# Kernel optimization log

Measured on AMD Instinct MI355X. Metric: run time of the kernel, lower is better.

Reference implementation:

```python
import jax, jax.numpy as jnp
import numpy as np

T, B, NS, NC = 100, 4096, 12, 4
N = NS + NC  # tau dim


def setup_inputs() -> dict:
    key = jax.random.key(0)
    k1, k2, k3, k4, k5 = jax.random.split(key, 5)
    # Symmetric PD quadratic cost C = L L^T / N + I  -> well conditioned
    L = jax.random.normal(k1, (T, B, N, N), dtype=jnp.float32) * 0.1
    C = jnp.einsum('tbij,tbkj->tbik', L, L) + jnp.eye(N, dtype=jnp.float32)
    c = jax.random.normal(k2, (T, B, N), dtype=jnp.float32)
    # Linear dynamics x' = F [x;u] + f, state block near identity for stability
    F = jax.random.normal(k3, (T - 1, B, NS, N), dtype=jnp.float32) * 0.02
    A0 = jnp.concatenate([0.99 * jnp.eye(NS, dtype=jnp.float32),
                          jnp.zeros((NS, NC), jnp.float32)], axis=-1)
    F = F + A0  # broadcast over (T-1, B)
    f = jax.random.normal(k4, (T - 1, B, NS), dtype=jnp.float32) * 0.01
    x_init = jax.random.normal(k5, (B, NS), dtype=jnp.float32)
    return {"x_init": x_init, "C": C, "c": c, "F": F, "f": f}


def _lqr_solve(x_init, C, c, F, f):
    ns = x_init.shape[-1]
    # Pad dynamics to length T (terminal step has no dynamics; V starts at 0
    # so the padded zero F/f contribute nothing).
    Fp = jnp.concatenate([F, jnp.zeros_like(F[:1])], axis=0)  # [T,B,ns,n]
    fp = jnp.concatenate([f, jnp.zeros_like(f[:1])], axis=0)  # [T,B,ns]

    def bwd_step(carry, inp):
        V, v = carry                      # [B,ns,ns], [B,ns]
        Ct, ct, Ft, ft = inp
        # Q = C + F^T V F ; q = c + F^T (V f + v)
        Q = Ct + jnp.einsum('bsi,bst,btj->bij', Ft, V, Ft)
        Vf = jnp.einsum('bst,bt->bs', V, ft) + v
        q = ct + jnp.einsum('bsi,bs->bi', Ft, Vf)
        Qxx, Qxu = Q[:, :ns, :ns], Q[:, :ns, ns:]
        Qux, Quu = Q[:, ns:, :ns], Q[:, ns:, ns:]
        qx, qu = q[:, :ns], q[:, ns:]
        # Joint solve for K = -Quu^{-1} Qux, k = -Quu^{-1} qu
        Kk = -jnp.linalg.solve(Quu, jnp.concatenate([Qux, qu[..., None]], axis=-1))
        K, k = Kk[..., :ns], Kk[..., ns]
        Vn = Qxx + jnp.einsum('bij,bjk->bik', Qxu, K)
        Vn = 0.5 * (Vn + jnp.swapaxes(Vn, -1, -2))
        vn = qx + jnp.einsum('bij,bj->bi', Qxu, k)
        return (Vn, vn), (K, k)

    V0 = jnp.zeros((x_init.shape[0], ns, ns), C.dtype)
    v0 = jnp.zeros((x_init.shape[0], ns), C.dtype)
    _, (Kr, kr) = jax.lax.scan(bwd_step, (V0, v0),
                               (C[::-1], c[::-1], Fp[::-1], fp[::-1]))
    K, k = Kr[::-1], kr[::-1]  # [T,B,nc,ns], [T,B,nc]

    def fwd_step(x, inp):
        Ct, ct, Ft, ft, Kt, kt = inp
        u = jnp.einsum('bij,bj->bi', Kt, x) + kt
        tau = jnp.concatenate([x, u], axis=-1)
        cost = 0.5 * jnp.einsum('bi,bij,bj->b', tau, Ct, tau) \
               + jnp.einsum('bi,bi->b', ct, tau)
        xn = jnp.einsum('bij,bj->bi', Ft, tau) + ft
        return xn, (x, u, cost)

    _, (xs, us, costs) = jax.lax.scan(fwd_step, x_init, (C, c, Fp, fp, K, k))
    return xs, us, jnp.sum(costs, axis=0)


def reference(x_init, C, c, F, f):
    # MPC with QuadCost + LinDx and no box constraints: the iLQR loop
    # converges in one exact LQR solve (Riccati backward + forward rollout).
    x, u, objs = _lqr_solve(x_init, C, c, F, f)
    return x, u, objs
```

## Files before the change

### kernel.cpp

```cpp
#include <hip/hip_runtime.h>
#include <hip/hip_fp16.h>

#define TT 100
#define BB 4096
#define GS 648


__device__ __forceinline__ void bar_lds(){
  asm volatile("" ::: "memory");
  asm volatile("s_waitcnt lgkmcnt(0)" ::: "memory");
  __builtin_amdgcn_s_barrier();
  asm volatile("" ::: "memory");
}

template<int KMODE>
__device__ __forceinline__ void storeK(void* wsv, size_t of, int l, float X0,float X1,float X2,float X3){
  if (KMODE==0){
    float* wsb=(float*)wsv + of*52;
    if (l<12)       ((float4*)wsb)[l]  = make_float4(X0,X1,X2,X3);
    else if (l==12) ((float4*)wsb)[12] = make_float4(X0,X1,X2,X3);
  } else {
    __half* wsb=(__half*)wsv + of*52;
    if (l<12){
      wsb[l*4+0]=__float2half(X0); wsb[l*4+1]=__float2half(X1);
      wsb[l*4+2]=__float2half(X2); wsb[l*4+3]=__float2half(X3);
    } else if (l==12){
      wsb[48]=__float2half(X0); wsb[49]=__float2half(X1);
      wsb[50]=__float2half(X2); wsb[51]=__float2half(X3);
    }
  }
}
template<int KMODE>
__device__ __forceinline__ float4 loadKcol(const void* wsv, size_t of, int l){
  if (KMODE==0) return ((const float4*)((const float*)wsv + of*52))[l];
  const __half* p=(const __half*)wsv + of*52 + l*4;
  return make_float4(__half2float(p[0]),__half2float(p[1]),__half2float(p[2]),__half2float(p[3]));
}
template<int KMODE>
__device__ __forceinline__ float loadkk(const void* wsv, size_t of, int r){
  if (KMODE==0) return ((const float*)wsv)[of*52+48+r];
  return __half2float(((const __half*)wsv)[of*52+48+r]);
}

template<int KMODE>
__global__ __launch_bounds__(256)
void lqr_fused(const float* __restrict__ xinit,
               const float* __restrict__ Cg,
               const float* __restrict__ cg,
               const float* __restrict__ Fg,
               const float* __restrict__ fg,
               float* __restrict__ out,
               void* __restrict__ wsv)
{
  __shared__ float smem[GS*16];
  const int tid = threadIdx.x;
  const int g = tid >> 4, l = tid & 15;
  const int b = blockIdx.x*16 + g;
  const int gb = (tid & 63) & ~15;

  float* __restrict__ V   = smem + (size_t)g*GS;
  float* __restrict__ Fl  = V + 144;
  float* __restrict__ S   = V + 384;
  float* __restrict__ Qxu = V + 528;
  float* __restrict__ Quu = V + 576;
  float* __restrict__ vv  = V + 592;
  float* __restrict__ tb  = V + 604;

  if (l < 12){
    #pragma unroll
    for (int i=0;i<12;i++) V[i*12+l]=0.f;
    vv[l]=0.f;
  }

  float4 sC0,sC1,sC2,sC3; float sc_;
  float4 sF0=make_float4(0,0,0,0),sF1=sF0,sF2=sF0,sF3=sF0; float sf_=0.f;
  {
    const size_t of = ((size_t)(TT-1)*BB + b);
    const float4* pc = (const float4*)(Cg + of*256 + l*16);
    sC0=pc[0];sC1=pc[1];sC2=pc[2];sC3=pc[3];
    sc_ = cg[of*16 + l];
  }

  for (int tt=TT-1; tt>=0; --tt){
    const bool hasF = (tt < TT-1);
    float4 C0=sC0,C1=sC1,C2=sC2,C3=sC3; float rc=sc_;
    float4 F0=sF0,F1=sF1,F2=sF2,F3=sF3; float rf=sf_;

    if (hasF && l<12){
      float4* q=(float4*)(Fl + l*20);
      q[0]=F0;q[1]=F1;q[2]=F2;q[3]=F3;
      tb[l]=rf;
    }
    bar_lds();

    if (tt>0){
      const size_t of = ((size_t)(tt-1)*BB + b);
      const float4* pc=(const float4*)(Cg + of*256 + l*16);
      sC0=pc[0];sC1=pc[1];sC2=pc[2];sC3=pc[3];
      sc_=cg[of*16+l];
      if (l<12){
        const float4* pf=(const float4*)(Fg + of*192 + l*16);
        sF0=pf[0];sF1=pf[1];sF2=pf[2];sF3=pf[3];
        sf_=fg[of*12+l];
      }
    }

    float Qc[16] = {C0.x,C0.y,C0.z,C0.w, C1.x,C1.y,C1.z,C1.w,
                    C2.x,C2.y,C2.z,C2.w, C3.x,C3.y,C3.z,C3.w};
    float qv = rc;

    if (hasF){
      float Ftj[12], W[12];
      #pragma unroll
      for (int s=0;s<12;s++) Ftj[s]=Fl[s*20+l];
      #pragma unroll
      for (int s=0;s<12;s++){
        const float4* vr=(const float4*)(V+s*12);
        float4 v0=vr[0],v1=vr[1],v2=vr[2];
        W[s]= v0.x*Ftj[0]+v0.y*Ftj[1]+v0.z*Ftj[2]+v0.w*Ftj[3]
            + v1.x*Ftj[4]+v1.y*Ftj[5]+v1.z*Ftj[6]+v1.w*Ftj[7]
            + v2.x*Ftj[8]+v2.y*Ftj[9]+v2.z*Ftj[10]+v2.w*Ftj[11];
      }
      #pragma unroll
      for (int s=0;s<12;s++){
        const float4* fr=(const float4*)(Fl + s*20);
        float4 f0=fr[0],f1=fr[1],f2=fr[2],f3=fr[3];
        float w=W[s];
        Qc[0]+=f0.x*w;  Qc[1]+=f0.y*w;  Qc[2]+=f0.z*w;  Qc[3]+=f0.w*w;
        Qc[4]+=f1.x*w;  Qc[5]+=f1.y*w;  Qc[6]+=f1.z*w;  Qc[7]+=f1.w*w;
        Qc[8]+=f2.x*w;  Qc[9]+=f2.y*w;  Qc[10]+=f2.z*w; Qc[11]+=f2.w*w;
        Qc[12]+=f3.x*w; Qc[13]+=f3.y*w; Qc[14]+=f3.z*w; Qc[15]+=f3.w*w;
      }
      #pragma unroll
      for (int t2=0;t2<12;t2++) qv += W[t2]*tb[t2];
      #pragma unroll
      for (int s=0;s<12;s++) qv += Ftj[s]*vv[s];
    }

    if (l>=12){
      const int cc=l-12;
      #pragma unroll
      for (int r=0;r<4;r++) Quu[cc*4+r]=Qc[12+r];
      #pragma unroll
      for (int i=0;i<12;i++) Qxu[cc*12+i]=Qc[i];
    }
    bar_lds();

    float qu0=__shfl(qv,gb+12,64),qu1=__shfl(qv,gb+13,64),
          qu2=__shfl(qv,gb+14,64),qu3=__shfl(qv,gb+15,64);
    float b0,b1,b2,b3;
    if (l<12){b0=-Qc[12];b1=-Qc[13];b2=-Qc[14];b3=-Qc[15];}
    else     {b0=-qu0;b1=-qu1;b2=-qu2;b3=-qu3;}

    float a00=Quu[0],a10=Quu[1],a20=Quu[2],a30=Quu[3];
    float a01=Quu[4],a11=Quu[5],a21=Quu[6],a31=Quu[7];
    float a02=Quu[8],a12=Quu[9],a22=Quu[10],a32=Quu[11];
    float a03=Quu[12],a13=Quu[13],a23=Quu[14],a33=Quu[15];

    float i0=1.0f/a00;
    float m10=a10*i0,m20=a20*i0,m30=a30*i0;
    a11-=m10*a01;a12-=m10*a02;a13-=m10*a03;b1-=m10*b0;
    a21-=m20*a01;a22-=m20*a02;a23-=m20*a03;b2-=m20*b0;
    a31-=m30*a01;a32-=m30*a02;a33-=m30*a03;b3-=m30*b0;
    float i1=1.0f/a11;
    float m21=a21*i1,m31=a31*i1;
    a22-=m21*a12;a23-=m21*a13;b2-=m21*b1;
    a32-=m31*a12;a33-=m31*a13;b3-=m31*b1;
    float i2=1.0f/a22;
    float m32=a32*i2;
    a33-=m32*a23;b3-=m32*b2;
    float X3=b3/a33;
    float X2=(b2-a23*X3)*i2;
    float X1=(b1-a12*X2-a13*X3)*i1;
    float X0=(b0-a01*X1-a02*X2-a03*X3)*i0;

    float k0=__shfl(X0,gb+12,64),k1=__shfl(X1,gb+12,64),
          k2=__shfl(X2,gb+12,64),k3=__shfl(X3,gb+12,64);

    storeK<KMODE>(wsv, (size_t)tt*BB+b, l, X0,X1,X2,X3);

    float Vn[12];
    if (l<12){
      #pragma unroll
      for (int i=0;i<12;i++) Vn[i]=Qc[i];
      #pragma unroll
      for (int r=0;r<4;r++){
        const float Xr=(r==0)?X0:(r==1)?X1:(r==2)?X2:X3;
        const float4* qx=(const float4*)(Qxu+r*12);
        float4 x0=qx[0],x1=qx[1],x2=qx[2];
        Vn[0]+=x0.x*Xr; Vn[1]+=x0.y*Xr; Vn[2]+=x0.z*Xr;  Vn[3]+=x0.w*Xr;
        Vn[4]+=x1.x*Xr; Vn[5]+=x1.y*Xr; Vn[6]+=x1.z*Xr;  Vn[7]+=x1.w*Xr;
        Vn[8]+=x2.x*Xr; Vn[9]+=x2.y*Xr; Vn[10]+=x2.z*Xr; Vn[11]+=x2.w*Xr;
      }
      #pragma unroll
      for (int i=0;i<12;i++) S[i*12+l]=Vn[i];
    }
    bar_lds();

    if (l<12){
      float vn = qv + Qxu[0+l]*k0 + Qxu[12+l]*k1 + Qxu[24+l]*k2 + Qxu[36+l]*k3;
      const float4* sr=(const float4*)(S + l*12);
      float4 r0=sr[0],r1=sr[1],r2=sr[2];
      V[0*12+l]=0.5f*(Vn[0]+r0.x);   V[1*12+l]=0.5f*(Vn[1]+r0.y);
      V[2*12+l]=0.5f*(Vn[2]+r0.z);   V[3*12+l]=0.5f*(Vn[3]+r0.w);
      V[4*12+l]=0.5f*(Vn[4]+r1.x);   V[5*12+l]=0.5f*(Vn[5]+r1.y);
      V[6*12+l]=0.5f*(Vn[6]+r1.z);   V[7*12+l]=0.5f*(Vn[7]+r1.w);
      V[8*12+l]=0.5f*(Vn[8]+r2.x);   V[9*12+l]=0.5f*(Vn[9]+r2.y);
      V[10*12+l]=0.5f*(Vn[10]+r2.z); V[11*12+l]=0.5f*(Vn[11]+r2.w);
      vv[l]=vn;
    }
  }

  asm volatile("s_waitcnt vmcnt(0)" ::: "memory");

  float xj = (l<12)? xinit[(size_t)b*12+l] : 0.f;
  double costacc=0.0;

  float4 sK=make_float4(0,0,0,0); float sk_=0.f;
  {
    const float4* pc=(const float4*)(Cg + (size_t)b*256 + l*16);
    sC0=pc[0];sC1=pc[1];sC2=pc[2];sC3=pc[3];
    sc_=cg[(size_t)b*16+l];
    if (l<12){
      const float4* pf=(const float4*)(Fg + (size_t)b*192 + l*16);
      sF0=pf[0];sF1=pf[1];sF2=pf[2];sF3=pf[3];
      sf_=fg[(size_t)b*12+l];
      sK=loadKcol<KMODE>(wsv,(size_t)b,l);
    } else {
      sk_=loadkk<KMODE>(wsv,(size_t)b,l-12);
    }
  }

  for (int t=0;t<TT;t++){
    float4 C0=sC0,C1=sC1,C2=sC2,C3=sC3; float rc=sc_;
    float4 F0=sF0,F1=sF1,F2=sF2,F3=sF3; float rf=sf_;
    float4 K4=sK; float kl=sk_;

    if (t+1<TT){
      const size_t of=((size_t)(t+1)*BB + b);
      const float4* pc=(const float4*)(Cg + of*256 + l*16);
      sC0=pc[0];sC1=pc[1];sC2=pc[2];sC3=pc[3];
      sc_=cg[of*16+l];
      if (l<12) sK=loadKcol<KMODE>(wsv,of,l);
      else      sk_=loadkk<KMODE>(wsv,of,l-12);
      if (t+1<TT-1 && l<12){
        const float4* pf=(const float4*)(Fg + of*192 + l*16);
        sF0=pf[0];sF1=pf[1];sF2=pf[2];sF3=pf[3];
        sf_=fg[of*12+l];
      }
    }

    float pr0=0.f,pr1=0.f,pr2=0.f,pr3=0.f;
    if (l<12){ pr0=K4.x*xj; pr1=K4.y*xj; pr2=K4.z*xj; pr3=K4.w*xj; }
    #pragma unroll
    for (int m=1;m<16;m<<=1){
      pr0+=__shfl_xor(pr0,m,64); pr1+=__shfl_xor(pr1,m,64);
      pr2+=__shfl_xor(pr2,m,64); pr3+=__shfl_xor(pr3,m,64);
    }
    float tauj;
    if (l<12) tauj=xj;
    else {
      float ur=(l==12)?pr0:(l==13)?pr1:(l==14)?pr2:pr3;
      tauj=ur+kl;
    }
    float* tbuf = tb + (t&1)*16;
    tbuf[l]=tauj;
    bar_lds();

    float4 t0=((const float4*)tbuf)[0], t1v=((const float4*)tbuf)[1],
           t2v=((const float4*)tbuf)[2], t3v=((const float4*)tbuf)[3];

    const float Cr[16]={C0.x,C0.y,C0.z,C0.w,C1.x,C1.y,C1.z,C1.w,
                        C2.x,C2.y,C2.z,C2.w,C3.x,C3.y,C3.z,C3.w};
    const float ta[16]={t0.x,t0.y,t0.z,t0.w,t1v.x,t1v.y,t1v.z,t1v.w,
                        t2v.x,t2v.y,t2v.z,t2v.w,t3v.x,t3v.y,t3v.z,t3v.w};
    float dot=0.f;
    #pragma unroll
    for (int j=0;j<16;j++) dot += Cr[j]*ta[j];
    costacc += (double)(tauj*(0.5f*dot+rc));

    if (l<12) out[(size_t)t*BB*12 + (size_t)b*12 + l] = xj;
    else      out[(size_t)TT*BB*12 + (size_t)t*BB*4 + (size_t)b*4 + (l-12)] = tauj;

    if (t<TT-1 && l<12){
      const float Fr[16]={F0.x,F0.y,F0.z,F0.w,F1.x,F1.y,F1.z,F1.w,
                          F2.x,F2.y,F2.z,F2.w,F3.x,F3.y,F3.z,F3.w};
      float d2=rf;
      #pragma unroll
      for (int j=0;j<16;j++) d2 += Fr[j]*ta[j];
      xj=d2;
    }
  }

  costacc+=__shfl_xor(costacc,1,64); costacc+=__shfl_xor(costacc,2,64);
  costacc+=__shfl_xor(costacc,4,64); costacc+=__shfl_xor(costacc,8,64);
  if (l==0) out[(size_t)TT*BB*16 + b]=(float)costacc;
}

extern "C" void kernel_launch(void* const* d_in, const int* in_sizes, int n_in,
                              void* d_out, int out_size, void* d_ws, size_t ws_size,
                              hipStream_t stream){
  (void)in_sizes; (void)n_in; (void)out_size;
  const float* xinit=(const float*)d_in[0];
  const float* C    =(const float*)d_in[1];
  const float* c    =(const float*)d_in[2];
  const float* F    =(const float*)d_in[3];
  const float* f    =(const float*)d_in[4];
  const size_t need_f32 = (size_t)TT*BB*52*sizeof(float);
  if (ws_size >= need_f32){
    lqr_fused<0><<<dim3(BB/16), dim3(256), 0, stream>>>(xinit,C,c,F,f,(float*)d_out,d_ws);
  } else {
    lqr_fused<1><<<dim3(BB/16), dim3(256), 0, stream>>>(xinit,C,c,F,f,(float*)d_out,d_ws);
  }
}
```

Baseline: 526.0 us.

## Split each batch item across 32 lanes and drop block barriers

Each batch element now gets 32 threads (two halves of 16) instead of 16. The F^T V F work, the Q row products and the V update are split across the halves and combined with cross-half shuffles. The grid doubles, and each wave now holds two batch items whose LDS regions never overlap, so the full s_barrier is replaced by an lgkmcnt wait. This is meant to shorten the serial per-step dependency chain and raise parallelism. In exchange the forward pass leaves half the lanes mostly idle and adds extra shuffles.

```diff
diff --git a/kernel.cpp b/kernel.cpp
--- a/kernel.cpp
+++ b/kernel.cpp
@@ -6,12 +6,7 @@
 #define GS 648
 
 
-__device__ __forceinline__ void bar_lds(){
-  asm volatile("" ::: "memory");
-  asm volatile("s_waitcnt lgkmcnt(0)" ::: "memory");
-  __builtin_amdgcn_s_barrier();
-  asm volatile("" ::: "memory");
-}
+#define FENCE() asm volatile("s_waitcnt lgkmcnt(0)" ::: "memory")
 
 template<int KMODE>
 __device__ __forceinline__ void storeK(void* wsv, size_t of, int l, float X0,float X1,float X2,float X3){
@@ -52,13 +47,16 @@
                float* __restrict__ out,
                void* __restrict__ wsv)
 {
-  __shared__ float smem[GS*16];
-  const int tid = threadIdx.x;
-  const int g = tid >> 4, l = tid & 15;
-  const int b = blockIdx.x*16 + g;
-  const int gb = (tid & 63) & ~15;
-
-  float* __restrict__ V   = smem + (size_t)g*GS;
+  __shared__ float smem[GS*8];
+  const int tid  = threadIdx.x;
+  const int gi   = tid >> 5;
+  const int lane = tid & 63;
+  const int l    = tid & 15;
+  const int h    = (tid >> 4) & 1;
+  const int b    = blockIdx.x*8 + gi;
+  const int gb32 = lane & ~31;
+
+  float* __restrict__ V   = smem + gi*GS;
   float* __restrict__ Fl  = V + 144;
   float* __restrict__ S   = V + 384;
   float* __restrict__ Qxu = V + 528;
@@ -66,88 +64,101 @@
   float* __restrict__ vv  = V + 592;
   float* __restrict__ tb  = V + 604;
 
-  if (l < 12){
+  if (h==0 && l<12){
     #pragma unroll
     for (int i=0;i<12;i++) V[i*12+l]=0.f;
     vv[l]=0.f;
   }
 
-  float4 sC0,sC1,sC2,sC3; float sc_;
-  float4 sF0=make_float4(0,0,0,0),sF1=sF0,sF2=sF0,sF3=sF0; float sf_=0.f;
+  float4 sCa,sCb; float sc_;
+  float4 sFa=make_float4(0,0,0,0),sFb=sFa; float sf_=0.f;
   {
     const size_t of = ((size_t)(TT-1)*BB + b);
     const float4* pc = (const float4*)(Cg + of*256 + l*16);
-    sC0=pc[0];sC1=pc[1];sC2=pc[2];sC3=pc[3];
+    sCa=pc[2*h]; sCb=pc[2*h+1];
     sc_ = cg[of*16 + l];
   }
 
   for (int tt=TT-1; tt>=0; --tt){
     const bool hasF = (tt < TT-1);
-    float4 C0=sC0,C1=sC1,C2=sC2,C3=sC3; float rc=sc_;
-    float4 F0=sF0,F1=sF1,F2=sF2,F3=sF3; float rf=sf_;
+    float4 Ca=sCa,Cb=sCb; float rc=sc_;
+    float4 Fa=sFa,Fb=sFb; float rf=sf_;
 
     if (hasF && l<12){
       float4* q=(float4*)(Fl + l*20);
-      q[0]=F0;q[1]=F1;q[2]=F2;q[3]=F3;
-      tb[l]=rf;
-    }
-    bar_lds();
+      q[2*h]=Fa; q[2*h+1]=Fb;
+      if (h==0) tb[l]=rf;
+    }
+    FENCE();
 
     if (tt>0){
       const size_t of = ((size_t)(tt-1)*BB + b);
       const float4* pc=(const float4*)(Cg + of*256 + l*16);
-      sC0=pc[0];sC1=pc[1];sC2=pc[2];sC3=pc[3];
+      sCa=pc[2*h]; sCb=pc[2*h+1];
       sc_=cg[of*16+l];
       if (l<12){
         const float4* pf=(const float4*)(Fg + of*192 + l*16);
-        sF0=pf[0];sF1=pf[1];sF2=pf[2];sF3=pf[3];
-        sf_=fg[of*12+l];
-      }
-    }
-
-    float Qc[16] = {C0.x,C0.y,C0.z,C0.w, C1.x,C1.y,C1.z,C1.w,
-                    C2.x,C2.y,C2.z,C2.w, C3.x,C3.y,C3.z,C3.w};
-    float qv = rc;
+        sFa=pf[2*h]; sFb=pf[2*h+1];
+        if (h==0) sf_=fg[of*12+l];
+      }
+    }
+
+    const float R0=Ca.x,R1=Ca.y,R2=Ca.z,R3=Ca.w,R4=Cb.x,R5=Cb.y,R6=Cb.z,R7=Cb.w;
+    float Qp[16];
+    Qp[0]=h?0.f:R0; Qp[1]=h?0.f:R1; Qp[2]=h?0.f:R2; Qp[3]=h?0.f:R3;
+    Qp[4]=h?0.f:R4; Qp[5]=h?0.f:R5; Qp[6]=h?0.f:R6; Qp[7]=h?0.f:R7;
+    Qp[8]=h?R0:0.f; Qp[9]=h?R1:0.f; Qp[10]=h?R2:0.f; Qp[11]=h?R3:0.f;
+    Qp[12]=h?R4:0.f; Qp[13]=h?R5:0.f; Qp[14]=h?R6:0.f; Qp[15]=h?R7:0.f;
+    float qvp = h? 0.f : rc;
 
     if (hasF){
-      float Ftj[12], W[12];
-      #pragma unroll
-      for (int s=0;s<12;s++) Ftj[s]=Fl[s*20+l];
-      #pragma unroll
-      for (int s=0;s<12;s++){
-        const float4* vr=(const float4*)(V+s*12);
+      float FtL[6], FtH[6];
+      #pragma unroll
+      for (int k2=0;k2<6;k2++){ FtL[k2]=Fl[k2*20+l]; FtH[k2]=Fl[(6+k2)*20+l]; }
+      const int s0=6*h;
+      float Wl[6];
+      #pragma unroll
+      for (int k2=0;k2<6;k2++){
+        const float4* vr=(const float4*)(V+(s0+k2)*12);
         float4 v0=vr[0],v1=vr[1],v2=vr[2];
-        W[s]= v0.x*Ftj[0]+v0.y*Ftj[1]+v0.z*Ftj[2]+v0.w*Ftj[3]
-            + v1.x*Ftj[4]+v1.y*Ftj[5]+v1.z*Ftj[6]+v1.w*Ftj[7]
-            + v2.x*Ftj[8]+v2.y*Ftj[9]+v2.z*Ftj[10]+v2.w*Ftj[11];
-      }
-      #pragma unroll
-      for (int s=0;s<12;s++){
-        const float4* fr=(const float4*)(Fl + s*20);
+        Wl[k2]= v0.x*FtL[0]+v0.y*FtL[1]+v0.z*FtL[2]+v0.w*FtL[3]
+              + v1.x*FtL[4]+v1.y*FtL[5]+v1.z*FtH[0]+v1.w*FtH[1]
+              + v2.x*FtH[2]+v2.y*FtH[3]+v2.z*FtH[4]+v2.w*FtH[5];
+      }
+      #pragma unroll
+      for (int k2=0;k2<6;k2++){
+        const float4* fr=(const float4*)(Fl + (s0+k2)*20);
         float4 f0=fr[0],f1=fr[1],f2=fr[2],f3=fr[3];
-        float w=W[s];
-        Qc[0]+=f0.x*w;  Qc[1]+=f0.y*w;  Qc[2]+=f0.z*w;  Qc[3]+=f0.w*w;
-        Qc[4]+=f1.x*w;  Qc[5]+=f1.y*w;  Qc[6]+=f1.z*w;  Qc[7]+=f1.w*w;
-        Qc[8]+=f2.x*w;  Qc[9]+=f2.y*w;  Qc[10]+=f2.z*w; Qc[11]+=f2.w*w;
-        Qc[12]+=f3.x*w; Qc[13]+=f3.y*w; Qc[14]+=f3.z*w; Qc[15]+=f3.w*w;
-      }
-      #pragma unroll
-      for (int t2=0;t2<12;t2++) qv += W[t2]*tb[t2];
-      #pragma unroll
-      for (int s=0;s<12;s++) qv += Ftj[s]*vv[s];
-    }
-
-    if (l>=12){
+        float w=Wl[k2];
+        Qp[0]+=f0.x*w;  Qp[1]+=f0.y*w;  Qp[2]+=f0.z*w;  Qp[3]+=f0.w*w;
+        Qp[4]+=f1.x*w;  Qp[5]+=f1.y*w;  Qp[6]+=f1.z*w;  Qp[7]+=f1.w*w;
+        Qp[8]+=f2.x*w;  Qp[9]+=f2.y*w;  Qp[10]+=f2.z*w; Qp[11]+=f2.w*w;
+        Qp[12]+=f3.x*w; Qp[13]+=f3.y*w; Qp[14]+=f3.z*w; Qp[15]+=f3.w*w;
+      }
+      #pragma unroll
+      for (int k2=0;k2<6;k2++){
+        qvp += Wl[k2]*tb[s0+k2];
+        const float ftk = h? FtH[k2] : FtL[k2];
+        qvp += ftk * vv[s0+k2];
+      }
+    }
+
+    float Qc[16];
+    #pragma unroll
+    for (int i=0;i<16;i++) Qc[i] = Qp[i] + __shfl_xor(Qp[i],16,64);
+    float qv = qvp + __shfl_xor(qvp,16,64);
+
+    if (h==0 && l>=12){
       const int cc=l-12;
       #pragma unroll
       for (int r=0;r<4;r++) Quu[cc*4+r]=Qc[12+r];
       #pragma unroll
       for (int i=0;i<12;i++) Qxu[cc*12+i]=Qc[i];
     }
-    bar_lds();
-
-    float qu0=__shfl(qv,gb+12,64),qu1=__shfl(qv,gb+13,64),
-          qu2=__shfl(qv,gb+14,64),qu3=__shfl(qv,gb+15,64);
+    FENCE();
+
+    float qu0=__shfl(qv,gb32+12,64),qu1=__shfl(qv,gb32+13,64),
+          qu2=__shfl(qv,gb32+14,64),qu3=__shfl(qv,gb32+15,64);
     float b0,b1,b2,b3;
     if (l<12){b0=-Qc[12];b1=-Qc[13];b2=-Qc[14];b3=-Qc[15];}
     else     {b0=-qu0;b1=-qu1;b2=-qu2;b3=-qu3;}
@@ -174,127 +185,123 @@
     float X1=(b1-a12*X2-a13*X3)*i1;
     float X0=(b0-a01*X1-a02*X2-a03*X3)*i0;
 
-    float k0=__shfl(X0,gb+12,64),k1=__shfl(X1,gb+12,64),
-          k2=__shfl(X2,gb+12,64),k3=__shfl(X3,gb+12,64);
-
-    storeK<KMODE>(wsv, (size_t)tt*BB+b, l, X0,X1,X2,X3);
-
-    float Vn[12];
+    if (h==0) storeK<KMODE>(wsv, (size_t)tt*BB+b, l, X0,X1,X2,X3);
+
+    const float k0=__shfl(X0,gb32+12,64),k1=__shfl(X1,gb32+12,64),
+                k2=__shfl(X2,gb32+12,64),k3=__shfl(X3,gb32+12,64);
+
+    float Vn[6];
     if (l<12){
-      #pragma unroll
-      for (int i=0;i<12;i++) Vn[i]=Qc[i];
-      #pragma unroll
-      for (int r=0;r<4;r++){
-        const float Xr=(r==0)?X0:(r==1)?X1:(r==2)?X2:X3;
-        const float4* qx=(const float4*)(Qxu+r*12);
-        float4 x0=qx[0],x1=qx[1],x2=qx[2];
-        Vn[0]+=x0.x*Xr; Vn[1]+=x0.y*Xr; Vn[2]+=x0.z*Xr;  Vn[3]+=x0.w*Xr;
-        Vn[4]+=x1.x*Xr; Vn[5]+=x1.y*Xr; Vn[6]+=x1.z*Xr;  Vn[7]+=x1.w*Xr;
-        Vn[8]+=x2.x*Xr; Vn[9]+=x2.y*Xr; Vn[10]+=x2.z*Xr; Vn[11]+=x2.w*Xr;
-      }
-      #pragma unroll
-      for (int i=0;i<12;i++) S[i*12+l]=Vn[i];
-    }
-    bar_lds();
-
+      const int i0i=6*h;
+      #pragma unroll
+      for (int k2=0;k2<6;k2++){
+        const int i=i0i+k2;
+        float vnk = h? Qc[6+k2] : Qc[k2];
+        vnk += Qxu[i]*X0 + Qxu[12+i]*X1 + Qxu[24+i]*X2 + Qxu[36+i]*X3;
+        S[i*12+l]=vnk; Vn[k2]=vnk;
+      }
+    }
+    FENCE();
     if (l<12){
-      float vn = qv + Qxu[0+l]*k0 + Qxu[12+l]*k1 + Qxu[24+l]*k2 + Qxu[36+l]*k3;
-      const float4* sr=(const float4*)(S + l*12);
-      float4 r0=sr[0],r1=sr[1],r2=sr[2];
-      V[0*12+l]=0.5f*(Vn[0]+r0.x);   V[1*12+l]=0.5f*(Vn[1]+r0.y);
-      V[2*12+l]=0.5f*(Vn[2]+r0.z);   V[3*12+l]=0.5f*(Vn[3]+r0.w);
-      V[4*12+l]=0.5f*(Vn[4]+r1.x);   V[5*12+l]=0.5f*(Vn[5]+r1.y);
-      V[6*12+l]=0.5f*(Vn[6]+r1.z);   V[7*12+l]=0.5f*(Vn[7]+r1.w);
-      V[8*12+l]=0.5f*(Vn[8]+r2.x);   V[9*12+l]=0.5f*(Vn[9]+r2.y);
-      V[10*12+l]=0.5f*(Vn[10]+r2.z); V[11*12+l]=0.5f*(Vn[11]+r2.w);
-      vv[l]=vn;
+      const int i0i=6*h;
+      #pragma unroll
+      for (int k2=0;k2<6;k2++){
+        const float sl=S[l*12 + i0i+k2];
+        V[(i0i+k2)*12+l]=0.5f*(Vn[k2]+sl);
+      }
+      if (h==0){
+        vv[l] = qv + Qxu[l]*k0 + Qxu[12+l]*k1 + Qxu[24+l]*k2 + Qxu[36+l]*k3;
+      }
     }
   }
 
   asm volatile("s_waitcnt vmcnt(0)" ::: "memory");
 
-  float xj = (l<12)? xinit[(size_t)b*12+l] : 0.f;
+  float xj = (h==0 && l<12)? xinit[(size_t)b*12+l] : 0.f;
   double costacc=0.0;
 
+  float4 sF0=make_float4(0,0,0,0),sF1=sF0,sF2=sF0,sF3=sF0;
   float4 sK=make_float4(0,0,0,0); float sk_=0.f;
   {
     const float4* pc=(const float4*)(Cg + (size_t)b*256 + l*16);
-    sC0=pc[0];sC1=pc[1];sC2=pc[2];sC3=pc[3];
+    sCa=pc[2*h]; sCb=pc[2*h+1];
     sc_=cg[(size_t)b*16+l];
-    if (l<12){
+    if (h==0 && l<12){
       const float4* pf=(const float4*)(Fg + (size_t)b*192 + l*16);
       sF0=pf[0];sF1=pf[1];sF2=pf[2];sF3=pf[3];
       sf_=fg[(size_t)b*12+l];
       sK=loadKcol<KMODE>(wsv,(size_t)b,l);
-    } else {
-      sk_=loadkk<KMODE>(wsv,(size_t)b,l-12);
-    }
+    }
+    if (h==0 && l>=12) sk_=loadkk<KMODE>(wsv,(size_t)b,l-12);
   }
 
   for (int t=0;t<TT;t++){
-    float4 C0=sC0,C1=sC1,C2=sC2,C3=sC3; float rc=sc_;
+    float4 Ca=sCa,Cb=sCb; float rc=sc_;
     float4 F0=sF0,F1=sF1,F2=sF2,F3=sF3; float rf=sf_;
     float4 K4=sK; float kl=sk_;
 
     if (t+1<TT){
       const size_t of=((size_t)(t+1)*BB + b);
       const float4* pc=(const float4*)(Cg + of*256 + l*16);
-      sC0=pc[0];sC1=pc[1];sC2=pc[2];sC3=pc[3];
+      sCa=pc[2*h]; sCb=pc[2*h+1];
       sc_=cg[of*16+l];
-      if (l<12) sK=loadKcol<KMODE>(wsv,of,l);
-      else      sk_=loadkk<KMODE>(wsv,of,l-12);
-      if (t+1<TT-1 && l<12){
-        const float4* pf=(const float4*)(Fg + of*192 + l*16);
-        sF0=pf[0];sF1=pf[1];sF2=pf[2];sF3=pf[3];
-        sf_=fg[of*12+l];
-      }
+      if (h==0 && l<12){
+        sK=loadKcol<KMODE>(wsv,of,l);
+        if (t+1<TT-1){
+          const float4* pf=(const float4*)(Fg + of*192 + l*16);
+          sF0=pf[0];sF1=pf[1];sF2=pf[2];sF3=pf[3];
+          sf_=fg[of*12+l];
+        }
+      }
+      if (h==0 && l>=12) sk_=loadkk<KMODE>(wsv,of,l-12);
     }
 
     float pr0=0.f,pr1=0.f,pr2=0.f,pr3=0.f;
-    if (l<12){ pr0=K4.x*xj; pr1=K4.y*xj; pr2=K4.z*xj; pr3=K4.w*xj; }
+    if (h==0 && l<12){ pr0=K4.x*xj; pr1=K4.y*xj; pr2=K4.z*xj; pr3=K4.w*xj; }
     #pragma unroll
     for (int m=1;m<16;m<<=1){
       pr0+=__shfl_xor(pr0,m,64); pr1+=__shfl_xor(pr1,m,64);
       pr2+=__shfl_xor(pr2,m,64); pr3+=__shfl_xor(pr3,m,64);
     }
-    float tauj;
-    if (l<12) tauj=xj;
-    else {
-      float ur=(l==12)?pr0:(l==13)?pr1:(l==14)?pr2:pr3;
-      tauj=ur+kl;
-    }
     float* tbuf = tb + (t&1)*16;
-    tbuf[l]=tauj;
-    bar_lds();
-
-    float4 t0=((const float4*)tbuf)[0], t1v=((const float4*)tbuf)[1],
-           t2v=((const float4*)tbuf)[2], t3v=((const float4*)tbuf)[3];
-
-    const float Cr[16]={C0.x,C0.y,C0.z,C0.w,C1.x,C1.y,C1.z,C1.w,
-                        C2.x,C2.y,C2.z,C2.w,C3.x,C3.y,C3.z,C3.w};
-    const float ta[16]={t0.x,t0.y,t0.z,t0.w,t1v.x,t1v.y,t1v.z,t1v.w,
-                        t2v.x,t2v.y,t2v.z,t2v.w,t3v.x,t3v.y,t3v.z,t3v.w};
-    float dot=0.f;
-    #pragma unroll
-    for (int j=0;j<16;j++) dot += Cr[j]*ta[j];
-    costacc += (double)(tauj*(0.5f*dot+rc));
-
-    if (l<12) out[(size_t)t*BB*12 + (size_t)b*12 + l] = xj;
-    else      out[(size_t)TT*BB*12 + (size_t)t*BB*4 + (size_t)b*4 + (l-12)] = tauj;
-
-    if (t<TT-1 && l<12){
-      const float Fr[16]={F0.x,F0.y,F0.z,F0.w,F1.x,F1.y,F1.z,F1.w,
-                          F2.x,F2.y,F2.z,F2.w,F3.x,F3.y,F3.z,F3.w};
-      float d2=rf;
-      #pragma unroll
-      for (int j=0;j<16;j++) d2 += Fr[j]*ta[j];
-      xj=d2;
+    float tauj=0.f;
+    if (h==0){
+      if (l<12) tauj=xj;
+      else {
+        const float ur=(l==12)?pr0:(l==13)?pr1:(l==14)?pr2:pr3;
+        tauj=ur+kl;
+      }
+      tbuf[l]=tauj;
+    }
+    FENCE();
+
+    const float4* tp=(const float4*)tbuf;
+    const float4 ta=tp[2*h], tb4=tp[2*h+1];
+    const float taul = tbuf[l];
+
+    float dot_p = Ca.x*ta.x + Ca.y*ta.y + Ca.z*ta.z + Ca.w*ta.w
+                + Cb.x*tb4.x + Cb.y*tb4.y + Cb.z*tb4.z + Cb.w*tb4.w;
+    costacc += (double)( taul*0.5f*dot_p + (h==0 ? taul*rc : 0.f) );
+
+    if (h==0){
+      if (l<12) out[(size_t)t*BB*12 + (size_t)b*12 + l] = xj;
+      else      out[(size_t)TT*BB*12 + (size_t)t*BB*4 + (size_t)b*4 + (l-12)] = tauj;
+    }
+
+    if (t<TT-1 && h==0 && l<12){
+      const float4 t0=tp[0],t1=tp[1],t2=tp[2],t3=tp[3];
+      xj = rf
+         + F0.x*t0.x+F0.y*t0.y+F0.z*t0.z+F0.w*t0.w
+         + F1.x*t1.x+F1.y*t1.y+F1.z*t1.z+F1.w*t1.w
+         + F2.x*t2.x+F2.y*t2.y+F2.z*t2.z+F2.w*t2.w
+         + F3.x*t3.x+F3.y*t3.y+F3.z*t3.z+F3.w*t3.w;
     }
   }
 
   costacc+=__shfl_xor(costacc,1,64); costacc+=__shfl_xor(costacc,2,64);
   costacc+=__shfl_xor(costacc,4,64); costacc+=__shfl_xor(costacc,8,64);
-  if (l==0) out[(size_t)TT*BB*16 + b]=(float)costacc;
+  costacc+=__shfl_xor(costacc,16,64);
+  if (h==0 && l==0) out[(size_t)TT*BB*16 + b]=(float)costacc;
 }
 
 extern "C" void kernel_launch(void* const* d_in, const int* in_sizes, int n_in,
@@ -308,8 +315,8 @@
   const float* f    =(const float*)d_in[4];
   const size_t need_f32 = (size_t)TT*BB*52*sizeof(float);
   if (ws_size >= need_f32){
-    lqr_fused<0><<<dim3(BB/16), dim3(256), 0, stream>>>(xinit,C,c,F,f,(float*)d_out,d_ws);
+    lqr_fused<0><<<dim3(BB/8), dim3(256), 0, stream>>>(xinit,C,c,F,f,(float*)d_out,d_ws);
   } else {
-    lqr_fused<1><<<dim3(BB/16), dim3(256), 0, stream>>>(xinit,C,c,F,f,(float*)d_out,d_ws);
-  }
-}
+    lqr_fused<1><<<dim3(BB/8), dim3(256), 0, stream>>>(xinit,C,c,F,f,(float*)d_out,d_ws);
+  }
+}
```

Measured after the change: 466.6 us. -11.3%, faster.
